# Kernel tuning notes

Measured on AMD Instinct MI355X. Metric: run time of the kernel, lower is better.

The kernel has to match this reference:

```python
import jax, jax.numpy as jnp
import numpy as np

N_HEADS = 4


def setup_inputs() -> dict:
    key = jax.random.key(0)
    k1, k2, k3 = jax.random.split(key, 3)
    B, C, H, W = 16, 512, 32, 32
    x = jax.random.normal(k1, (B, C, H, W), dtype=jnp.float32)
    # Linear weights stored as (in, out) so y = x @ w + b
    w_proj = jax.random.normal(k2, (C, 3 * C), dtype=jnp.float32) * (C ** -0.5)
    b_proj = jnp.zeros((3 * C,), dtype=jnp.float32)
    w_out = jax.random.normal(k3, (C, C), dtype=jnp.float32) * (C ** -0.5)
    b_out = jnp.zeros((C,), dtype=jnp.float32)
    return {"x": x, "w_proj": w_proj, "b_proj": b_proj, "w_out": w_out, "b_out": b_out}


def reference(x, w_proj, b_proj, w_out, b_out):
    B, C, H, W = x.shape
    d_k = C // N_HEADS
    scale = d_k ** -0.5
    # NOTE: original module defines GroupNorm but never applies it in forward.
    xf = x.reshape(B, C, H * W).transpose(0, 2, 1)          # (B, N, C)
    qkv = xf @ w_proj + b_proj                                # (B, N, 3C)
    qkv = qkv.reshape(B, -1, N_HEADS, 3 * d_k)
    q, k, v = jnp.split(qkv, 3, axis=-1)                      # each (B, N, H, d_k)
    attn = jnp.einsum('bihd,bjhd->bijh', q, k) * scale        # (B, N, N, H)
    attn = jax.nn.softmax(attn, axis=2)                       # softmax over j
    res = jnp.einsum('bijh,bjhd->bihd', attn, v)              # (B, N, H, d_k)
    res = res.reshape(B, -1, N_HEADS * d_k)                   # (B, N, C)
    res = res @ w_out + b_out + xf                            # residual add
    return res.transpose(0, 2, 1).reshape(B, C, H, W)
```

## Files before the change

kernel.cpp:

```cpp
#include <hip/hip_runtime.h>

#define B_  16
#define C_  512
#define N_  1024
#define NH  4
#define DK  128
#define M3  1536

typedef unsigned short u16;
typedef unsigned int   u32;
typedef __attribute__((ext_vector_type(8))) short bfrag;
typedef __attribute__((ext_vector_type(4))) float f4;

#define MFMA(a, b, c) __builtin_amdgcn_mfma_f32_16x16x32_bf16(a, b, c, 0, 0, 0)

#define GL2LDS(gp, lp) __builtin_amdgcn_global_load_lds( \
    (__attribute__((address_space(1))) const unsigned int*)(const void*)(gp), \
    (__attribute__((address_space(3))) unsigned int*)(void*)(lp), 16, 0, 0)

__device__ __forceinline__ u16 f2bf(float f) {
    u32 u = __float_as_uint(f);
    return (u16)((u + 0x7FFFu + ((u >> 16) & 1u)) >> 16);
}
__device__ __forceinline__ float bf2f(u16 h) { return __uint_as_float(((u32)h) << 16); }

#define QSCL 0.12751741859316937f

__global__ __launch_bounds__(256) void conv_split_t(
    const float* __restrict__ src, u16* __restrict__ dhi, u16* __restrict__ dlo,
    int R, int Cc)
{
    __shared__ float Ts[64][65];
    const int tid = threadIdx.x;
    const int c0 = blockIdx.x * 64, r0 = blockIdx.y * 64;
    const size_t bofs = (size_t)blockIdx.z * R * Cc;

#pragma unroll
    for (int p = 0; p < 4; ++p) {
        int r = p * 16 + (tid >> 4);
        int c = (tid & 15) * 4;
        float4 v = *(const float4*)(src + bofs + (size_t)(r0 + r) * Cc + c0 + c);
        Ts[c + 0][r] = v.x; Ts[c + 1][r] = v.y; Ts[c + 2][r] = v.z; Ts[c + 3][r] = v.w;
    }
    __syncthreads();
#pragma unroll
    for (int p = 0; p < 4; ++p) {
        int cc = p * 16 + (tid >> 4);
        int rr = (tid & 15) * 4;
        float f0 = Ts[cc][rr + 0], f1 = Ts[cc][rr + 1];
        float f2 = Ts[cc][rr + 2], f3 = Ts[cc][rr + 3];
        u16 h0 = f2bf(f0), h1 = f2bf(f1), h2 = f2bf(f2), h3 = f2bf(f3);
        u16 l0 = f2bf(f0 - bf2f(h0)), l1 = f2bf(f1 - bf2f(h1));
        u16 l2 = f2bf(f2 - bf2f(h2)), l3 = f2bf(f3 - bf2f(h3));
        size_t o = bofs + (size_t)(c0 + cc) * R + r0 + rr;
        *(uint2*)(void*)(dhi + o) = make_uint2((u32)h0 | ((u32)h1 << 16), (u32)h2 | ((u32)h3 << 16));
        *(uint2*)(void*)(dlo + o) = make_uint2((u32)l0 | ((u32)l1 << 16), (u32)l2 | ((u32)l3 << 16));
    }
}

__global__ __launch_bounds__(256, 2) void qkv_mfma(
    const u16* __restrict__ xt_hi, const u16* __restrict__ xt_lo,
    const u16* __restrict__ wpT_hi, const u16* __restrict__ wpT_lo,
    const float* __restrict__ bp,
    u16* __restrict__ Qh, u16* __restrict__ Ql,
    u16* __restrict__ Kh, u16* __restrict__ Kl,
    u16* __restrict__ Vth, u16* __restrict__ Vtl)
{
    __shared__ __align__(16) u16 AH[128 * 64], AL[128 * 64], BH[128 * 64], BL[128 * 64];
    const int tid = threadIdx.x;
    const int l = tid & 63, w = tid >> 6;
    const int wr = w >> 1, wc = w & 1;
    const int lm = l & 15, kg = l >> 4;
    const int bx = blockIdx.x, by = blockIdx.y, b = blockIdx.z;
    const int m0 = bx * 128, n0 = by * 128;

    const u16* gsrc =
        (w == 0) ? xt_hi + ((size_t)b * N_ + n0) * C_ :
        (w == 1) ? xt_lo + ((size_t)b * N_ + n0) * C_ :
        (w == 2) ? wpT_hi + (size_t)m0 * C_ :
                   wpT_lo + (size_t)m0 * C_;
    u16* ldst = (w == 0) ? AH : (w == 1) ? AL : (w == 2) ? BH : BL;
    const int lane_off = (l >> 3) * C_ + (((l & 7) ^ (l >> 3)) << 3);

    f4 acc[4][4] = {};

    for (int it = 0; it < 8; ++it) {
        __syncthreads();
        const u16* g = gsrc + it * 64 + lane_off;
#pragma unroll
        for (int u = 0; u < 16; ++u)
            GL2LDS(g + (size_t)u * 8 * C_, ldst + u * 512);
        __syncthreads();

#pragma unroll
        for (int kk = 0; kk < 2; ++kk) {
            bfrag ah[4], al[4], bh[4], bl[4];
            const int s = ((kk * 4 + kg) ^ (lm & 7)) << 3;
#pragma unroll
            for (int f = 0; f < 4; ++f) {
                const int ar = wr * 64 + f * 16 + lm;
                const int br = wc * 64 + f * 16 + lm;
                ah[f] = *(const bfrag*)(AH + ar * 64 + s);
                al[f] = *(const bfrag*)(AL + ar * 64 + s);
                bh[f] = *(const bfrag*)(BH + br * 64 + s);
                bl[f] = *(const bfrag*)(BL + br * 64 + s);
            }
#pragma unroll
            for (int i = 0; i < 4; ++i)
#pragma unroll
                for (int j = 0; j < 4; ++j) {
                    acc[i][j] = MFMA(ah[i], bh[j], acc[i][j]);
                    acc[i][j] = MFMA(ah[i], bl[j], acc[i][j]);
                    acc[i][j] = MFMA(al[i], bh[j], acc[i][j]);
                }
        }
    }

    const int hh = bx / 3, t = bx - hh * 3;
#pragma unroll
    for (int j = 0; j < 4; ++j) {
        const int mcol = m0 + wc * 64 + j * 16 + lm;
        const float bias = bp[mcol];
        const int d = mcol & 127;
#pragma unroll
        for (int i = 0; i < 4; ++i) {
            const int tok = n0 + wr * 64 + i * 16 + kg * 4;
            if (t == 2) {
                u16 hb[4], lb[4];
#pragma unroll
                for (int r = 0; r < 4; ++r) {
                    float v = acc[i][j][r] + bias;
                    hb[r] = f2bf(v);
                    lb[r] = f2bf(v - bf2f(hb[r]));
                }
                const size_t o = ((size_t)(b * NH + hh) * DK + d) * N_ + tok;
                *(uint2*)(void*)(Vth + o) = make_uint2((u32)hb[0] | ((u32)hb[1] << 16),
                                                       (u32)hb[2] | ((u32)hb[3] << 16));
                *(uint2*)(void*)(Vtl + o) = make_uint2((u32)lb[0] | ((u32)lb[1] << 16),
                                                       (u32)lb[2] | ((u32)lb[3] << 16));
            } else {
                u16* dh = (t == 0) ? Qh : Kh;
                u16* dl = (t == 0) ? Ql : Kl;
                const size_t o = ((size_t)(b * NH + hh) * N_ + tok) * DK + d;
#pragma unroll
                for (int r = 0; r < 4; ++r) {
                    float v = acc[i][j][r] + bias;
                    if (t == 0) v *= QSCL;
                    u16 hb = f2bf(v);
                    dh[o + (size_t)r * DK] = hb;
                    dl[o + (size_t)r * DK] = f2bf(v - bf2f(hb));
                }
            }
        }
    }
}

__global__ __launch_bounds__(512, 2) void attn_mfma(
    const u16* __restrict__ Qh_, const u16* __restrict__ Ql_,
    const u16* __restrict__ Kh_, const u16* __restrict__ Kl_,
    const u16* __restrict__ Vth_, const u16* __restrict__ Vtl_,
    u16* __restrict__ res_hi, u16* __restrict__ res_lo)
{
    __shared__ __align__(16) u16 KH[64 * 128], KL[64 * 128];
    __shared__ __align__(16) u16 VH[128 * 64], VL[128 * 64];
    __shared__ u16 Ph[8][16][72], Pl[8][16][72];

    const int tid = threadIdx.x;
    const int l = tid & 63, w = tid >> 6;
    const int lm = l & 15, kg = l >> 4;
    const int bh = blockIdx.x;
    const int qc = blockIdx.y;
    const int i = qc * 128 + w * 16 + lm;
    const size_t head = (size_t)bh * N_ * DK;

    const u16* sgK = (w & 2) ? Kl_ : Kh_;
    const u16* sgV = (w & 2) ? Vtl_ : Vth_;
    u16* sdK = (w & 2) ? KL : KH;
    u16* sdV = (w & 2) ? VL : VH;
    const int sub0 = (w & 1) * 8;

    bfrag qfh[4], qfl[4];
    {
        const u16* qp = Qh_ + head + (size_t)i * DK + kg * 8;
        const u16* qp2 = Ql_ + head + (size_t)i * DK + kg * 8;
#pragma unroll
        for (int kc = 0; kc < 4; ++kc) {
            qfh[kc] = *(const bfrag*)(qp + kc * 32);
            qfl[kc] = *(const bfrag*)(qp2 + kc * 32);
        }
    }

    f4 acc_o[8] = {};
    float m_r = -3.0e38f, l_r = 0.f;

    for (int jt = 0; jt < 16; ++jt) {
        __syncthreads();
        if (w < 4) {
#pragma unroll
            for (int u = 0; u < 8; ++u) {
                const int rbase = (sub0 + u) * 4;
                const int row = rbase + (l >> 4);
                GL2LDS(sgK + head + (size_t)(jt * 64 + row) * DK + (((l & 15) ^ (row & 7)) << 3),
                       sdK + rbase * 128);
            }
        } else {
#pragma unroll
            for (int u = 0; u < 8; ++u) {
                const int rbase = (sub0 + u) * 8;
                const int row = rbase + (l >> 3);
                GL2LDS(sgV + (size_t)bh * DK * N_ + (size_t)row * N_ + jt * 64
                           + (((l & 7) ^ (row & 7)) << 3),
                       sdV + rbase * 64);
            }
        }
        __syncthreads();

        f4 sacc[4] = {};
#pragma unroll
        for (int kc = 0; kc < 4; ++kc) {
#pragma unroll
            for (int jf = 0; jf < 4; ++jf) {
                const int row = jf * 16 + lm;
                const int sw = (((kc << 2) | kg) ^ (lm & 7)) << 3;
                bfrag kh = *(const bfrag*)(KH + row * 128 + sw);
                bfrag kl = *(const bfrag*)(KL + row * 128 + sw);
                sacc[jf] = MFMA(kh, qfh[kc], sacc[jf]);
                sacc[jf] = MFMA(kh, qfl[kc], sacc[jf]);
                sacc[jf] = MFMA(kl, qfh[kc], sacc[jf]);
            }
        }

        float mt = sacc[0][0];
#pragma unroll
        for (int jf = 0; jf < 4; ++jf)
#pragma unroll
            for (int r = 0; r < 4; ++r) mt = fmaxf(mt, sacc[jf][r]);
        mt = fmaxf(mt, __shfl_xor(mt, 16));
        mt = fmaxf(mt, __shfl_xor(mt, 32));
        const float mn = fmaxf(m_r, mt);
        const float alpha = exp2f(m_r - mn);
        m_r = mn;

        float p[16];
        float rs = 0.f;
#pragma unroll
        for (int jf = 0; jf < 4; ++jf)
#pragma unroll
            for (int r = 0; r < 4; ++r) {
                float pv = exp2f(sacc[jf][r] - mn);
                p[jf * 4 + r] = pv;
                rs += pv;
            }
        rs += __shfl_xor(rs, 16);
        rs += __shfl_xor(rs, 32);
        l_r = l_r * alpha + rs;
#pragma unroll
        for (int df = 0; df < 8; ++df)
#pragma unroll
            for (int r = 0; r < 4; ++r) acc_o[df][r] *= alpha;

#pragma unroll
        for (int jf = 0; jf < 4; ++jf) {
            u16 hb[4], lb[4];
#pragma unroll
            for (int r = 0; r < 4; ++r) {
                float pv = p[jf * 4 + r];
                hb[r] = f2bf(pv);
                lb[r] = f2bf(pv - bf2f(hb[r]));
            }
            *(uint2*)(void*)&Ph[w][lm][jf * 16 + kg * 4] =
                make_uint2((u32)hb[0] | ((u32)hb[1] << 16), (u32)hb[2] | ((u32)hb[3] << 16));
            *(uint2*)(void*)&Pl[w][lm][jf * 16 + kg * 4] =
                make_uint2((u32)lb[0] | ((u32)lb[1] << 16), (u32)lb[2] | ((u32)lb[3] << 16));
        }

#pragma unroll
        for (int kc2 = 0; kc2 < 2; ++kc2) {
            bfrag pbh = *(const bfrag*)&Ph[w][lm][kc2 * 32 + kg * 8];
            bfrag pbl = *(const bfrag*)&Pl[w][lm][kc2 * 32 + kg * 8];
#pragma unroll
            for (int df = 0; df < 8; ++df) {
                const int row = df * 16 + lm;
                const int sw = (((kc2 << 2) | kg) ^ (lm & 7)) << 3;
                bfrag vh = *(const bfrag*)(VH + row * 64 + sw);
                bfrag vl = *(const bfrag*)(VL + row * 64 + sw);
                acc_o[df] = MFMA(vh, pbh, acc_o[df]);
                acc_o[df] = MFMA(vh, pbl, acc_o[df]);
                acc_o[df] = MFMA(vl, pbh, acc_o[df]);
            }
        }
    }

    const float inv = 1.f / l_r;
    const int b = bh >> 2, h = bh & 3;
    const size_t ro = ((size_t)b * N_ + i) * C_ + h * DK;
#pragma unroll
    for (int df = 0; df < 8; ++df) {
        u16 hb[4], lb[4];
#pragma unroll
        for (int r = 0; r < 4; ++r) {
            float v = acc_o[df][r] * inv;
            hb[r] = f2bf(v);
            lb[r] = f2bf(v - bf2f(hb[r]));
        }
        const size_t o = ro + df * 16 + kg * 4;
        *(uint2*)(void*)(res_hi + o) = make_uint2((u32)hb[0] | ((u32)hb[1] << 16),
                                                  (u32)hb[2] | ((u32)hb[3] << 16));
        *(uint2*)(void*)(res_lo + o) = make_uint2((u32)lb[0] | ((u32)lb[1] << 16),
                                                  (u32)lb[2] | ((u32)lb[3] << 16));
    }
}

__global__ __launch_bounds__(256, 2) void out_mfma(
    const u16* __restrict__ woT_hi, const u16* __restrict__ woT_lo,
    const u16* __restrict__ res_hi, const u16* __restrict__ res_lo,
    const float* __restrict__ bo, const float* __restrict__ x,
    float* __restrict__ out)
{
    __shared__ __align__(16) u16 AH[128 * 64], AL[128 * 64], BH[128 * 64], BL[128 * 64];
    const int tid = threadIdx.x;
    const int l = tid & 63, w = tid >> 6;
    const int wr = w >> 1, wc = w & 1;
    const int lm = l & 15, kg = l >> 4;
    const int bx = blockIdx.x, by = blockIdx.y, b = blockIdx.z;
    const int c0 = bx * 128, n0 = by * 128;

    const u16* gsrc =
        (w == 0) ? woT_hi + (size_t)c0 * C_ :
        (w == 1) ? woT_lo + (size_t)c0 * C_ :
        (w == 2) ? res_hi + ((size_t)b * N_ + n0) * C_ :
                   res_lo + ((size_t)b * N_ + n0) * C_;
    u16* ldst = (w == 0) ? AH : (w == 1) ? AL : (w == 2) ? BH : BL;
    const int lane_off = (l >> 3) * C_ + (((l & 7) ^ (l >> 3)) << 3);

    f4 acc[4][4] = {};

    for (int it = 0; it < 8; ++it) {
        __syncthreads();
        const u16* g = gsrc + it * 64 + lane_off;
#pragma unroll
        for (int u = 0; u < 16; ++u)
            GL2LDS(g + (size_t)u * 8 * C_, ldst + u * 512);
        __syncthreads();

#pragma unroll
        for (int kk = 0; kk < 2; ++kk) {
            bfrag ah[4], al[4], bh[4], bl[4];
            const int s = ((kk * 4 + kg) ^ (lm & 7)) << 3;
#pragma unroll
            for (int f = 0; f < 4; ++f) {
                const int ar = wr * 64 + f * 16 + lm;
                const int br = wc * 64 + f * 16 + lm;
                ah[f] = *(const bfrag*)(AH + ar * 64 + s);
                al[f] = *(const bfrag*)(AL + ar * 64 + s);
                bh[f] = *(const bfrag*)(BH + br * 64 + s);
                bl[f] = *(const bfrag*)(BL + br * 64 + s);
            }
#pragma unroll
            for (int i = 0; i < 4; ++i)
#pragma unroll
                for (int j = 0; j < 4; ++j) {
                    acc[i][j] = MFMA(ah[i], bh[j], acc[i][j]);
                    acc[i][j] = MFMA(ah[i], bl[j], acc[i][j]);
                    acc[i][j] = MFMA(al[i], bh[j], acc[i][j]);
                }
        }
    }

#pragma unroll
    for (int j = 0; j < 4; ++j) {
        const int ncol = n0 + wc * 64 + j * 16 + lm;
#pragma unroll
        for (int i = 0; i < 4; ++i) {
#pragma unroll
            for (int r = 0; r < 4; ++r) {
                const int crow = c0 + wr * 64 + i * 16 + kg * 4 + r;
                const size_t o = ((size_t)b * C_ + crow) * N_ + ncol;
                out[o] = acc[i][j][r] + bo[crow] + x[o];
            }
        }
    }
}

extern "C" void kernel_launch(void* const* d_in, const int* in_sizes, int n_in,
                              void* d_out, int out_size, void* d_ws, size_t ws_size,
                              hipStream_t stream) {
    const float* x  = (const float*)d_in[0];
    const float* wp = (const float*)d_in[1];
    const float* bp = (const float*)d_in[2];
    const float* wo = (const float*)d_in[3];
    const float* bo = (const float*)d_in[4];
    float* out = (float*)d_out;

    const size_t SEG = (size_t)B_ * N_ * C_;
    u16* xt_hi = (u16*)d_ws;
    u16* xt_lo = xt_hi + SEG;
    u16* Qh  = xt_hi + 2 * SEG;
    u16* Ql  = Qh + SEG;
    u16* Kh  = Ql + SEG;
    u16* Kl  = Kh + SEG;
    u16* Vth = Kl + SEG;
    u16* Vtl = Vth + SEG;
    u16* res_hi = xt_hi;
    u16* res_lo = xt_lo;
    u16* woT_hi = Qh;
    u16* woT_lo = woT_hi + C_ * C_;
    u16* wpT_hi = (u16*)d_out;
    u16* wpT_lo = wpT_hi + C_ * M3;

    conv_split_t<<<dim3(16, 8, 16), 256, 0, stream>>>(x, xt_hi, xt_lo, C_, N_);
    conv_split_t<<<dim3(24, 8, 1), 256, 0, stream>>>(wp, wpT_hi, wpT_lo, C_, M3);
    qkv_mfma<<<dim3(12, 8, 16), 256, 0, stream>>>(xt_hi, xt_lo, wpT_hi, wpT_lo, bp,
                                                  Qh, Ql, Kh, Kl, Vth, Vtl);
    attn_mfma<<<dim3(64, 8), 512, 0, stream>>>(Qh, Ql, Kh, Kl, Vth, Vtl, res_hi, res_lo);
    conv_split_t<<<dim3(8, 8, 1), 256, 0, stream>>>(wo, woT_hi, woT_lo, C_, C_);
    out_mfma<<<dim3(4, 8, 16), 256, 0, stream>>>(woT_hi, woT_lo, res_hi, res_lo, bo, x, out);
}
```

Before: 359.0 us.

## Process two query sub-tiles per wave in attention to reuse K/V tiles

Each wave now handles two 16-row query sub-tiles, so a block covers 256 queries and the grid halves. Every K/V tile loaded into LDS and every K/V fragment read from LDS feeds twice as many MFMAs. This cuts global K/V reload traffic and LDS reads per unit of work. In exchange, register use roughly doubles for accumulators and Q fragments, and fewer blocks are launched, which risks spills and lower occupancy.

```diff
diff --git a/kernel.cpp b/kernel.cpp
--- a/kernel.cpp
+++ b/kernel.cpp
@@ -163,14 +163,14 @@
 {
     __shared__ __align__(16) u16 KH[64 * 128], KL[64 * 128];
     __shared__ __align__(16) u16 VH[128 * 64], VL[128 * 64];
-    __shared__ u16 Ph[8][16][72], Pl[8][16][72];
+    __shared__ u16 Ph[8][2][16][72], Pl[8][2][16][72];
 
     const int tid = threadIdx.x;
     const int l = tid & 63, w = tid >> 6;
     const int lm = l & 15, kg = l >> 4;
     const int bh = blockIdx.x;
     const int qc = blockIdx.y;
-    const int i = qc * 128 + w * 16 + lm;
+    const int i0s = qc * 256 + w * 16 + lm;
     const size_t head = (size_t)bh * N_ * DK;
 
     const u16* sgK = (w & 2) ? Kl_ : Kh_;
@@ -179,19 +179,20 @@
     u16* sdV = (w & 2) ? VL : VH;
     const int sub0 = (w & 1) * 8;
 
-    bfrag qfh[4], qfl[4];
-    {
-        const u16* qp = Qh_ + head + (size_t)i * DK + kg * 8;
-        const u16* qp2 = Ql_ + head + (size_t)i * DK + kg * 8;
+    bfrag qfh[2][4], qfl[2][4];
+#pragma unroll
+    for (int s = 0; s < 2; ++s) {
+        const u16* qp  = Qh_ + head + (size_t)(i0s + s * 128) * DK + kg * 8;
+        const u16* qp2 = Ql_ + head + (size_t)(i0s + s * 128) * DK + kg * 8;
 #pragma unroll
         for (int kc = 0; kc < 4; ++kc) {
-            qfh[kc] = *(const bfrag*)(qp + kc * 32);
-            qfl[kc] = *(const bfrag*)(qp2 + kc * 32);
-        }
-    }
-
-    f4 acc_o[8] = {};
-    float m_r = -3.0e38f, l_r = 0.f;
+            qfh[s][kc] = *(const bfrag*)(qp + kc * 32);
+            qfl[s][kc] = *(const bfrag*)(qp2 + kc * 32);
+        }
+    }
+
+    f4 acc_o[2][8] = {};
+    float m_r[2] = {-3.0e38f, -3.0e38f}, l_r[2] = {0.f, 0.f};
 
     for (int jt = 0; jt < 16; ++jt) {
         __syncthreads();
@@ -215,7 +216,7 @@
         }
         __syncthreads();
 
-        f4 sacc[4] = {};
+        f4 sacc[2][4] = {};
 #pragma unroll
         for (int kc = 0; kc < 4; ++kc) {
 #pragma unroll
@@ -224,90 +225,95 @@
                 const int sw = (((kc << 2) | kg) ^ (lm & 7)) << 3;
                 bfrag kh = *(const bfrag*)(KH + row * 128 + sw);
                 bfrag kl = *(const bfrag*)(KL + row * 128 + sw);
-                sacc[jf] = MFMA(kh, qfh[kc], sacc[jf]);
-                sacc[jf] = MFMA(kh, qfl[kc], sacc[jf]);
-                sacc[jf] = MFMA(kl, qfh[kc], sacc[jf]);
-            }
-        }
-
-        float mt = sacc[0][0];
-#pragma unroll
-        for (int jf = 0; jf < 4; ++jf)
-#pragma unroll
-            for (int r = 0; r < 4; ++r) mt = fmaxf(mt, sacc[jf][r]);
-        mt = fmaxf(mt, __shfl_xor(mt, 16));
-        mt = fmaxf(mt, __shfl_xor(mt, 32));
-        const float mn = fmaxf(m_r, mt);
-        const float alpha = exp2f(m_r - mn);
-        m_r = mn;
-
-        float p[16];
-        float rs = 0.f;
-#pragma unroll
-        for (int jf = 0; jf < 4; ++jf)
-#pragma unroll
-            for (int r = 0; r < 4; ++r) {
-                float pv = exp2f(sacc[jf][r] - mn);
-                p[jf * 4 + r] = pv;
-                rs += pv;
-            }
-        rs += __shfl_xor(rs, 16);
-        rs += __shfl_xor(rs, 32);
-        l_r = l_r * alpha + rs;
-#pragma unroll
-        for (int df = 0; df < 8; ++df)
-#pragma unroll
-            for (int r = 0; r < 4; ++r) acc_o[df][r] *= alpha;
-
-#pragma unroll
-        for (int jf = 0; jf < 4; ++jf) {
-            u16 hb[4], lb[4];
-#pragma unroll
-            for (int r = 0; r < 4; ++r) {
-                float pv = p[jf * 4 + r];
-                hb[r] = f2bf(pv);
-                lb[r] = f2bf(pv - bf2f(hb[r]));
-            }
-            *(uint2*)(void*)&Ph[w][lm][jf * 16 + kg * 4] =
-                make_uint2((u32)hb[0] | ((u32)hb[1] << 16), (u32)hb[2] | ((u32)hb[3] << 16));
-            *(uint2*)(void*)&Pl[w][lm][jf * 16 + kg * 4] =
-                make_uint2((u32)lb[0] | ((u32)lb[1] << 16), (u32)lb[2] | ((u32)lb[3] << 16));
+#pragma unroll
+                for (int s = 0; s < 2; ++s) {
+                    sacc[s][jf] = MFMA(kh, qfh[s][kc], sacc[s][jf]);
+                    sacc[s][jf] = MFMA(kh, qfl[s][kc], sacc[s][jf]);
+                    sacc[s][jf] = MFMA(kl, qfh[s][kc], sacc[s][jf]);
+                }
+            }
+        }
+
+#pragma unroll
+        for (int s = 0; s < 2; ++s) {
+            float mt = sacc[s][0][0];
+#pragma unroll
+            for (int jf = 0; jf < 4; ++jf)
+#pragma unroll
+                for (int r = 0; r < 4; ++r) mt = fmaxf(mt, sacc[s][jf][r]);
+            mt = fmaxf(mt, __shfl_xor(mt, 16));
+            mt = fmaxf(mt, __shfl_xor(mt, 32));
+            const float mn = fmaxf(m_r[s], mt);
+            const float alpha = exp2f(m_r[s] - mn);
+            m_r[s] = mn;
+
+            float rs = 0.f;
+#pragma unroll
+            for (int jf = 0; jf < 4; ++jf) {
+                u16 hb[4], lb[4];
+#pragma unroll
+                for (int r = 0; r < 4; ++r) {
+                    float pv = exp2f(sacc[s][jf][r] - mn);
+                    rs += pv;
+                    hb[r] = f2bf(pv);
+                    lb[r] = f2bf(pv - bf2f(hb[r]));
+                }
+                *(uint2*)(void*)&Ph[w][s][lm][jf * 16 + kg * 4] =
+                    make_uint2((u32)hb[0] | ((u32)hb[1] << 16), (u32)hb[2] | ((u32)hb[3] << 16));
+                *(uint2*)(void*)&Pl[w][s][lm][jf * 16 + kg * 4] =
+                    make_uint2((u32)lb[0] | ((u32)lb[1] << 16), (u32)lb[2] | ((u32)lb[3] << 16));
+            }
+            rs += __shfl_xor(rs, 16);
+            rs += __shfl_xor(rs, 32);
+            l_r[s] = l_r[s] * alpha + rs;
+#pragma unroll
+            for (int df = 0; df < 8; ++df)
+#pragma unroll
+                for (int r = 0; r < 4; ++r) acc_o[s][df][r] *= alpha;
         }
 
 #pragma unroll
         for (int kc2 = 0; kc2 < 2; ++kc2) {
-            bfrag pbh = *(const bfrag*)&Ph[w][lm][kc2 * 32 + kg * 8];
-            bfrag pbl = *(const bfrag*)&Pl[w][lm][kc2 * 32 + kg * 8];
+            bfrag pbh0 = *(const bfrag*)&Ph[w][0][lm][kc2 * 32 + kg * 8];
+            bfrag pbl0 = *(const bfrag*)&Pl[w][0][lm][kc2 * 32 + kg * 8];
+            bfrag pbh1 = *(const bfrag*)&Ph[w][1][lm][kc2 * 32 + kg * 8];
+            bfrag pbl1 = *(const bfrag*)&Pl[w][1][lm][kc2 * 32 + kg * 8];
 #pragma unroll
             for (int df = 0; df < 8; ++df) {
                 const int row = df * 16 + lm;
                 const int sw = (((kc2 << 2) | kg) ^ (lm & 7)) << 3;
                 bfrag vh = *(const bfrag*)(VH + row * 64 + sw);
                 bfrag vl = *(const bfrag*)(VL + row * 64 + sw);
-                acc_o[df] = MFMA(vh, pbh, acc_o[df]);
-                acc_o[df] = MFMA(vh, pbl, acc_o[df]);
-                acc_o[df] = MFMA(vl, pbh, acc_o[df]);
-            }
-        }
-    }
-
-    const float inv = 1.f / l_r;
+                acc_o[0][df] = MFMA(vh, pbh0, acc_o[0][df]);
+                acc_o[0][df] = MFMA(vh, pbl0, acc_o[0][df]);
+                acc_o[0][df] = MFMA(vl, pbh0, acc_o[0][df]);
+                acc_o[1][df] = MFMA(vh, pbh1, acc_o[1][df]);
+                acc_o[1][df] = MFMA(vh, pbl1, acc_o[1][df]);
+                acc_o[1][df] = MFMA(vl, pbh1, acc_o[1][df]);
+            }
+        }
+    }
+
     const int b = bh >> 2, h = bh & 3;
-    const size_t ro = ((size_t)b * N_ + i) * C_ + h * DK;
-#pragma unroll
-    for (int df = 0; df < 8; ++df) {
-        u16 hb[4], lb[4];
-#pragma unroll
-        for (int r = 0; r < 4; ++r) {
-            float v = acc_o[df][r] * inv;
-            hb[r] = f2bf(v);
-            lb[r] = f2bf(v - bf2f(hb[r]));
-        }
-        const size_t o = ro + df * 16 + kg * 4;
-        *(uint2*)(void*)(res_hi + o) = make_uint2((u32)hb[0] | ((u32)hb[1] << 16),
-                                                  (u32)hb[2] | ((u32)hb[3] << 16));
-        *(uint2*)(void*)(res_lo + o) = make_uint2((u32)lb[0] | ((u32)lb[1] << 16),
-                                                  (u32)lb[2] | ((u32)lb[3] << 16));
+#pragma unroll
+    for (int s = 0; s < 2; ++s) {
+        const float inv = 1.f / l_r[s];
+        const size_t ro = ((size_t)b * N_ + i0s + s * 128) * C_ + h * DK;
+#pragma unroll
+        for (int df = 0; df < 8; ++df) {
+            u16 hb[4], lb[4];
+#pragma unroll
+            for (int r = 0; r < 4; ++r) {
+                float v = acc_o[s][df][r] * inv;
+                hb[r] = f2bf(v);
+                lb[r] = f2bf(v - bf2f(hb[r]));
+            }
+            const size_t o = ro + df * 16 + kg * 4;
+            *(uint2*)(void*)(res_hi + o) = make_uint2((u32)hb[0] | ((u32)hb[1] << 16),
+                                                      (u32)hb[2] | ((u32)hb[3] << 16));
+            *(uint2*)(void*)(res_lo + o) = make_uint2((u32)lb[0] | ((u32)lb[1] << 16),
+                                                      (u32)lb[2] | ((u32)lb[3] << 16));
+        }
     }
 }
 
@@ -412,7 +418,7 @@
     conv_split_t<<<dim3(24, 8, 1), 256, 0, stream>>>(wp, wpT_hi, wpT_lo, C_, M3);
     qkv_mfma<<<dim3(12, 8, 16), 256, 0, stream>>>(xt_hi, xt_lo, wpT_hi, wpT_lo, bp,
                                                   Qh, Ql, Kh, Kl, Vth, Vtl);
-    attn_mfma<<<dim3(64, 8), 512, 0, stream>>>(Qh, Ql, Kh, Kl, Vth, Vtl, res_hi, res_lo);
+    attn_mfma<<<dim3(64, 4), 512, 0, stream>>>(Qh, Ql, Kh, Kl, Vth, Vtl, res_hi, res_lo);
     conv_split_t<<<dim3(8, 8, 1), 256, 0, stream>>>(wo, woT_hi, woT_lo, C_, C_);
     out_mfma<<<dim3(4, 8, 16), 256, 0, stream>>>(woT_hi, woT_lo, res_hi, res_lo, bo, x, out);
 }
```

Result: faster. 334.6 us (-6.8%).
